# Kernel optimization log

Measured on AMD Instinct MI355X. Metric: run time of the kernel, lower is better.

The kernel has to match this reference:

```python
import jax, jax.numpy as jnp
import numpy as np

B = 50000      # batch of graphs
NOBJ = 7       # tangram pieces per graph
HID = 64
EMB = 32
SIGMA = 25.0   # VE-SDE sigma for marginal_prob_std


def _lin_init(k, fin, fout):
    kw, kb = jax.random.split(k)
    s = 1.0 / np.sqrt(fin)
    w = jax.random.uniform(kw, (fin, fout), minval=-s, maxval=s, dtype=jnp.float32)
    b = jax.random.uniform(kb, (fout,), minval=-s, maxval=s, dtype=jnp.float32)
    return w, b


def setup_inputs() -> dict:
    key = jax.random.key(0)
    ks = jax.random.split(key, 16)
    N = B * NOBJ
    omega = jax.random.normal(ks[0], (N, 3), dtype=jnp.float32)
    t = jax.random.uniform(ks[1], (B, 1), minval=1e-3, maxval=1.0, dtype=jnp.float32)
    # fully-connected edges (no self loops) per graph, offset by graph index
    a, b = np.meshgrid(np.arange(NOBJ), np.arange(NOBJ), indexing='ij')
    m = a != b
    src0, dst0 = a[m], b[m]                       # (42,)
    offs = (np.arange(B) * NOBJ)[:, None]         # (B,1)
    src = (src0[None, :] + offs).reshape(-1)
    dst = (dst0[None, :] + offs).reshape(-1)
    edge_index = jnp.asarray(np.stack([src, dst]), dtype=jnp.int32)  # (2, B*42)
    W_fourier = jax.random.normal(ks[2], (EMB // 2,), dtype=jnp.float32) * 30.0
    wi1, bi1 = _lin_init(ks[3], 3, HID)
    wi2, bi2 = _lin_init(ks[4], HID, HID)
    wt, bt = _lin_init(ks[5], EMB, EMB)
    w1a, b1a = _lin_init(ks[6], HID * 2, HID)
    w1b, b1b = _lin_init(ks[7], HID, HID)
    w2a, b2a = _lin_init(ks[8], (HID + EMB) * 2, HID)
    w2b, b2b = _lin_init(ks[9], HID, HID)
    w3a, b3a = _lin_init(ks[10], (HID + EMB) * 2, HID)
    w3b, b3b = _lin_init(ks[11], HID, 3)
    return dict(omega=omega, edge_index=edge_index, t=t, num_objs=NOBJ,
                W_fourier=W_fourier,
                wi1=wi1, bi1=bi1, wi2=wi2, bi2=bi2, wt=wt, bt=bt,
                w1a=w1a, b1a=b1a, w1b=w1b, b1b=b1b,
                w2a=w2a, b2a=b2a, w2b=w2b, b2b=b2b,
                w3a=w3a, b3a=b3a, w3b=w3b, b3b=b3b)


def _mlp(x, wa, ba, wb, bb):
    return jax.nn.relu(x @ wa + ba) @ wb + bb


def reference(omega, edge_index, t, num_objs, W_fourier,
              wi1, bi1, wi2, bi2, wt, bt,
              w1a, b1a, w1b, b1b, w2a, b2a, w2b, b2b, w3a, b3a, w3b, b3b):
    N = omega.shape[0]
    src, dst = edge_index[0], edge_index[1]

    def edge_conv(x, wa, ba, wb, bb):
        # EdgeConv: msg = mlp([x_i, x_j - x_i]); max-aggregate at target i
        xi = x[dst]
        msg = _mlp(jnp.concatenate([xi, x[src] - xi], axis=-1), wa, ba, wb, bb)
        return jax.ops.segment_max(msg, dst, num_segments=N)

    init_feature = _mlp(omega, wi1, bi1, wi2, bi2)          # (N, HID)
    # Gaussian Fourier time embedding -> ReLU -> Linear -> ReLU
    proj = t[:, 0][:, None] * W_fourier[None, :] * (2.0 * jnp.pi)   # (B, EMB/2)
    emb = jnp.concatenate([jnp.sin(proj), jnp.cos(proj)], axis=-1)  # (B, EMB)
    xs = jax.nn.relu(jax.nn.relu(emb) @ wt + bt)                    # (B, EMB)
    # torch: xs.repeat(1, num_objs, 1).view(B*num_objs, -1) == tile whole block
    x_sigma = jnp.tile(xs, (num_objs, 1))                           # (N, EMB)

    x = jax.nn.relu(edge_conv(init_feature, w1a, b1a, w1b, b1b))
    x = jnp.concatenate([x, x_sigma], axis=-1)
    x = jax.nn.relu(edge_conv(x, w2a, b2a, w2b, b2b))
    x = jnp.concatenate([x, x_sigma], axis=-1)
    x = edge_conv(x, w3a, b3a, w3b, b3b)                            # (N, 3)

    # torch: t.repeat(1, num_objs).view(B*num_objs, -1) == repeat_interleave
    t_r = jnp.repeat(t, num_objs, axis=0)                           # (N, 1)
    std = jnp.sqrt((SIGMA ** (2.0 * t_r) - 1.0) / (2.0 * jnp.log(SIGMA)))
    return x / (std + 1e-7)
```

## Files before the change

kernel.cpp:

```cpp
#include <hip/hip_runtime.h>


#define NB 50000

typedef unsigned short u16;
typedef short short8 __attribute__((ext_vector_type(8)));
typedef float f32x4 __attribute__((ext_vector_type(4)));

#define OFF_I  0
#define OFF_1A 8192
#define OFF_2A 24576
#define OFF_3A 49152
#define OFF_1B 73728
#define OFF_2B 81920
#define OFF_WT 90112
#define OFF_3B 92160

#define HSTR 144
#define HLO  2304
#define XS2S 72
#define XS2LO 1152
#define SSTR 264
#define WREG 11136

__device__ __forceinline__ float b2f(u16 u) {
    return __uint_as_float(((unsigned int)u) << 16);
}
__device__ __forceinline__ u16 f2b(float f) {
    unsigned int u = __float_as_uint(f);
    u += 0x7FFFu + ((u >> 16) & 1u);
    return (u16)(u >> 16);
}
__device__ __forceinline__ float bcast(float v, int l) {
    return __uint_as_float(__builtin_amdgcn_readlane(__float_as_uint(v), l));
}

__global__ __launch_bounds__(128) void pack_kernel(
    const float* __restrict__ wi2, const float* __restrict__ w1a,
    const float* __restrict__ w2a, const float* __restrict__ w3a,
    const float* __restrict__ w1b, const float* __restrict__ w2b,
    const float* __restrict__ wt,  const float* __restrict__ w3b,
    u16* __restrict__ ws)
{
    int blk = blockIdx.x;
    int half = threadIdx.x >> 6;
    int lane = threadIdx.x & 63;
    if (blk < 88) {
        const float* src; int NT, qoff, obase, frag;
        if (blk < 8)       { src = wi2; NT = 4; qoff = 0;  obase = OFF_I;  frag = blk;      }
        else if (blk < 24) { src = w1a; NT = 8; qoff = 64; obase = OFF_1A; frag = blk - 8;  }
        else if (blk < 48) { src = w2a; NT = 8; qoff = 96; obase = OFF_2A; frag = blk - 24; }
        else if (blk < 72) { src = w3a; NT = 8; qoff = 96; obase = OFF_3A; frag = blk - 48; }
        else if (blk < 80) { src = w1b; NT = 4; qoff = 0;  obase = OFF_1B; frag = blk - 72; }
        else               { src = w2b; NT = 4; qoff = 0;  obase = OFF_2B; frag = blk - 80; }
        int kt = frag / NT, nt = frag % NT;
        int k0 = kt * 32 + (lane >> 4) * 8;
        int n  = nt * 16 + (lane & 15);
        u16* dst = ws + obase + frag * 1024 + half * 512 + lane * 8;
#pragma unroll
        for (int j = 0; j < 8; ++j) {
            int k = k0 + j;
            int idx = (n < 64) ? (k * 64 + n) : ((qoff + k) * 64 + (n - 64));
            float v = src[idx];
            u16 hi = f2b(v);
            dst[j] = (half == 0) ? hi : f2b(v - b2f(hi));
        }
    } else if (blk < 90) {
        int frag = blk - 88;
        int k0 = (lane >> 4) * 8;
        int n  = frag * 16 + (lane & 15);
        u16* dst = ws + OFF_WT + frag * 1024 + half * 512 + lane * 8;
#pragma unroll
        for (int j = 0; j < 8; ++j) {
            float v = wt[(k0 + j) * 32 + n];
            u16 hi = f2b(v);
            dst[j] = (half == 0) ? hi : f2b(v - b2f(hi));
        }
    } else {
        int frag = blk - 90;
        int k0 = frag * 32 + (lane >> 4) * 8;
        int n  = lane & 15;
        u16* dst = ws + OFF_3B + frag * 1024 + half * 512 + lane * 8;
#pragma unroll
        for (int j = 0; j < 8; ++j) {
            float v = (n < 3) ? w3b[(k0 + j) * 3 + n] : 0.f;
            u16 hi = f2b(v);
            dst[j] = (half == 0) ? hi : f2b(v - b2f(hi));
        }
    }
}

__device__ __forceinline__ f32x4 mfma3(short8 ah, short8 al, short8 bh, short8 bl, f32x4 acc) {
    acc = __builtin_amdgcn_mfma_f32_16x16x32_bf16(ah, bh, acc, 0, 0, 0);
    acc = __builtin_amdgcn_mfma_f32_16x16x32_bf16(ah, bl, acc, 0, 0, 0);
    acc = __builtin_amdgcn_mfma_f32_16x16x32_bf16(al, bh, acc, 0, 0, 0);
    return acc;
}

#define ROW(k) ((k) < 7 ? (k) : (k) + 1)

__device__ __forceinline__ void writeX64_14(char* W, int L, const float* v) {
#pragma unroll
    for (int k = 0; k < 14; ++k) {
        int r = ROW(k);
        u16 hi = f2b(v[k]);
        *(u16*)(W + r * HSTR + L * 2) = hi;
        *(u16*)(W + HLO + r * HSTR + L * 2) = f2b(v[k] - b2f(hi));
    }
}
template<int KT>
__device__ __forceinline__ void loadA(const char* W, const char* XS2, int L,
                                      short8* Ah, short8* Al) {
#pragma unroll
    for (int kt = 0; kt < KT; ++kt) {
        if (kt < 2) {
            Ah[kt] = *(const short8*)(W + (L & 15) * HSTR + kt * 64 + (L >> 4) * 16);
            Al[kt] = *(const short8*)(W + HLO + (L & 15) * HSTR + kt * 64 + (L >> 4) * 16);
        } else {
            Ah[kt] = *(const short8*)(XS2 + (L & 15) * XS2S + (L >> 4) * 16);
            Al[kt] = *(const short8*)(XS2 + XS2LO + (L & 15) * XS2S + (L >> 4) * 16);
        }
    }
}
template<int KT, int NT>
__device__ __forceinline__ void lin_pass(const u16* __restrict__ ws, int off, int nt0,
                                         const short8* Ah, const short8* Al,
                                         char* Sb, int L) {
#pragma unroll
    for (int ntc = 0; ntc < 4; ++ntc) {
        f32x4 acc = {0.f, 0.f, 0.f, 0.f};
#pragma unroll
        for (int kt = 0; kt < KT; ++kt) {
            int f = kt * NT + nt0 + ntc;
            short8 bh = *(const short8*)(ws + off + f * 1024 + L * 8);
            short8 bl = *(const short8*)(ws + off + f * 1024 + 512 + L * 8);
            acc = mfma3(Ah[kt], Al[kt], bh, bl, acc);
        }
#pragma unroll
        for (int rr = 0; rr < 4; ++rr)
            *(float*)(Sb + ((L >> 4) * 4 + rr) * SSTR + ntc * 64 + (L & 15) * 4) = acc[rr];
    }
}
__device__ __forceinline__ void readS14(const char* Sb, int L, float* o) {
#pragma unroll
    for (int k = 0; k < 14; ++k) o[k] = *(const float*)(Sb + ROW(k) * SSTR + L * 4);
}
__device__ __forceinline__ void stageH2(char* W, int c, const float* pp, const float* qq, int L) {
#pragma unroll
    for (int r = 0; r < 16; ++r) {
        int e = c * 16 + r;
        if (e < 84) {
            int gb = (e >= 42) ? 1 : 0;
            int el = e - gb * 42;
            int i = el / 6, jj = el - i * 6;
            int j = jj + (jj >= i);
            float hv = fmaxf(pp[gb * 7 + i] + qq[gb * 7 + j], 0.f);
            u16 hi = f2b(hv);
            *(u16*)(W + r * HSTR + L * 2) = hi;
            *(u16*)(W + HLO + r * HSTR + L * 2) = f2b(hv - b2f(hi));
        }
    }
}
__device__ __forceinline__ void loadAH(const char* W, int L,
                                       short8& Ah0, short8& Ah1, short8& Al0, short8& Al1) {
    Ah0 = *(const short8*)(W + (L & 15) * HSTR + (L >> 4) * 16);
    Ah1 = *(const short8*)(W + (L & 15) * HSTR + 64 + (L >> 4) * 16);
    Al0 = *(const short8*)(W + HLO + (L & 15) * HSTR + (L >> 4) * 16);
    Al1 = *(const short8*)(W + HLO + (L & 15) * HSTR + 64 + (L >> 4) * 16);
}

__device__ __forceinline__ void edgeconv2(const u16* __restrict__ ws, int offB,
                                          char* W, char* Sb,
                                          const float* pp, const float* qq,
                                          float vb, int L) {
    float mx[14];
#pragma unroll
    for (int k = 0; k < 14; ++k) mx[k] = -3.0e38f;
#pragma unroll
    for (int c = 0; c < 6; ++c) {
        stageH2(W, c, pp, qq, L);
        short8 Ah0, Ah1, Al0, Al1;
        loadAH(W, L, Ah0, Ah1, Al0, Al1);
#pragma unroll
        for (int nt = 0; nt < 4; ++nt) {
            short8 bh0 = *(const short8*)(ws + offB + nt * 1024 + L * 8);
            short8 bl0 = *(const short8*)(ws + offB + nt * 1024 + 512 + L * 8);
            short8 bh1 = *(const short8*)(ws + offB + (4 + nt) * 1024 + L * 8);
            short8 bl1 = *(const short8*)(ws + offB + (4 + nt) * 1024 + 512 + L * 8);
            f32x4 acc = {0.f, 0.f, 0.f, 0.f};
            acc = mfma3(Ah0, Al0, bh0, bl0, acc);
            acc = mfma3(Ah1, Al1, bh1, bl1, acc);
#pragma unroll
            for (int rr = 0; rr < 4; ++rr)
                *(float*)(Sb + ((L >> 4) * 4 + rr) * SSTR + nt * 64 + (L & 15) * 4) = acc[rr];
        }
#pragma unroll
        for (int r = 0; r < 16; ++r) {
            int e = c * 16 + r;
            if (e < 84) {
                int gb = (e >= 42) ? 1 : 0;
                int i = (e - gb * 42) / 6;
                float sv = *(const float*)(Sb + r * SSTR + L * 4);
                mx[gb * 7 + i] = fmaxf(mx[gb * 7 + i], sv);
            }
        }
    }
    float xo[14];
#pragma unroll
    for (int k = 0; k < 14; ++k) xo[k] = fmaxf(mx[k] + vb, 0.f);
    writeX64_14(W, L, xo);
}

__global__ __launch_bounds__(128) void gnn_kernel(
    const float* __restrict__ omega, const float* __restrict__ tt, const float* __restrict__ Wf,
    const float* __restrict__ wi1, const float* __restrict__ bi1, const float* __restrict__ bi2,
    const float* __restrict__ bt,
    const float* __restrict__ b1a, const float* __restrict__ b1b,
    const float* __restrict__ b2a, const float* __restrict__ b2b,
    const float* __restrict__ b3a, const float* __restrict__ b3b,
    const u16* __restrict__ ws, float* __restrict__ out)
{
    __shared__ __align__(16) char smem[2 * WREG];
    const int L   = threadIdx.x & 63;
    const int wav = threadIdx.x >> 6;
    const int p   = blockIdx.x * 2 + wav;
    const int g0  = p * 2;
    const int base0 = g0 * 7;
    char* W   = smem + wav * WREG;
    char* XS2 = W + 4608;
    char* Sb  = W + 6912;

    float omv = (L < 42) ? omega[base0 * 3 + L] : 0.f;
    float vwi10 = wi1[L], vwi11 = wi1[64 + L], vwi12 = wi1[128 + L];
    float vbi1 = bi1[L];
    float h1[14];
#pragma unroll
    for (int k = 0; k < 14; ++k) {
        float a0 = bcast(omv, 3 * k), a1 = bcast(omv, 3 * k + 1), a2 = bcast(omv, 3 * k + 2);
        h1[k] = fmaxf(fmaf(a0, vwi10, fmaf(a1, vwi11, fmaf(a2, vwi12, vbi1))), 0.f);
    }

    {
        int cc = L & 31;
        float vwf = Wf[cc & 15] * 6.283185307179586f;
        int tb = base0 - (base0 / NB) * NB;
#pragma unroll
        for (int k = 0; k < 14; ++k) {
            int ti = tb + k; if (ti >= NB) ti -= NB;
            float pj = tt[ti] * vwf;
            float remb = fmaxf((cc < 16) ? sinf(pj) : cosf(pj), 0.f);
            u16 hi = f2b(remb);
            if (L < 32) *(u16*)(W + ROW(k) * HSTR + cc * 2) = hi;
            else *(u16*)(W + HLO + ROW(k) * HSTR + cc * 2) = f2b(remb - b2f(hi));
        }
        short8 Eh = *(const short8*)(W + (L & 15) * HSTR + (L >> 4) * 16);
        short8 El = *(const short8*)(W + HLO + (L & 15) * HSTR + (L >> 4) * 16);
#pragma unroll
        for (int nt = 0; nt < 2; ++nt) {
            short8 bh = *(const short8*)(ws + OFF_WT + nt * 1024 + L * 8);
            short8 bl = *(const short8*)(ws + OFF_WT + nt * 1024 + 512 + L * 8);
            f32x4 acc = {0.f, 0.f, 0.f, 0.f};
            acc = mfma3(Eh, El, bh, bl, acc);
#pragma unroll
            for (int rr = 0; rr < 4; ++rr)
                *(float*)(Sb + ((L >> 4) * 4 + rr) * SSTR + nt * 64 + (L & 15) * 4) = acc[rr];
        }
        float vbt = bt[cc];
#pragma unroll
        for (int k = 0; k < 14; ++k) {
            float xv = fmaxf(*(const float*)(Sb + ROW(k) * SSTR + cc * 4) + vbt, 0.f);
            u16 hi = f2b(xv);
            if (L < 32) *(u16*)(XS2 + ROW(k) * XS2S + cc * 2) = hi;
            else *(u16*)(XS2 + XS2LO + ROW(k) * XS2S + cc * 2) = f2b(xv - b2f(hi));
        }
    }

    short8 Ah[3], Al[3];
    float pp[14], qq[14];

    writeX64_14(W, L, h1);
    loadA<2>(W, XS2, L, Ah, Al);
    lin_pass<2, 4>(ws, OFF_I, 0, Ah, Al, Sb, L);
    {
        float xh[14];
        readS14(Sb, L, xh);
        float vbi2 = bi2[L];
#pragma unroll
        for (int k = 0; k < 14; ++k) xh[k] += vbi2;
        writeX64_14(W, L, xh);
    }

    loadA<2>(W, XS2, L, Ah, Al);
    lin_pass<2, 8>(ws, OFF_1A, 0, Ah, Al, Sb, L);
    readS14(Sb, L, pp);
    lin_pass<2, 8>(ws, OFF_1A, 4, Ah, Al, Sb, L);
    readS14(Sb, L, qq);
    float vb1a = b1a[L];
#pragma unroll
    for (int k = 0; k < 14; ++k) pp[k] = pp[k] + vb1a - qq[k];
    edgeconv2(ws, OFF_1B, W, Sb, pp, qq, b1b[L], L);

    loadA<3>(W, XS2, L, Ah, Al);
    lin_pass<3, 8>(ws, OFF_2A, 0, Ah, Al, Sb, L);
    readS14(Sb, L, pp);
    lin_pass<3, 8>(ws, OFF_2A, 4, Ah, Al, Sb, L);
    readS14(Sb, L, qq);
    float vb2a = b2a[L];
#pragma unroll
    for (int k = 0; k < 14; ++k) pp[k] = pp[k] + vb2a - qq[k];
    edgeconv2(ws, OFF_2B, W, Sb, pp, qq, b2b[L], L);

    loadA<3>(W, XS2, L, Ah, Al);
    lin_pass<3, 8>(ws, OFF_3A, 0, Ah, Al, Sb, L);
    readS14(Sb, L, pp);
    lin_pass<3, 8>(ws, OFF_3A, 4, Ah, Al, Sb, L);
    readS14(Sb, L, qq);
    float vb3a = b3a[L];
#pragma unroll
    for (int k = 0; k < 14; ++k) pp[k] = pp[k] + vb3a - qq[k];

    {
        short8 B0h = *(const short8*)(ws + OFF_3B + L * 8);
        short8 B0l = *(const short8*)(ws + OFF_3B + 512 + L * 8);
        short8 B1h = *(const short8*)(ws + OFF_3B + 1024 + L * 8);
        short8 B1l = *(const short8*)(ws + OFF_3B + 1536 + L * 8);
#pragma unroll
        for (int c = 0; c < 6; ++c) {
            stageH2(W, c, pp, qq, L);
            short8 Ah0, Ah1, Al0, Al1;
            loadAH(W, L, Ah0, Ah1, Al0, Al1);
            f32x4 acc = {0.f, 0.f, 0.f, 0.f};
            acc = mfma3(Ah0, Al0, B0h, B0l, acc);
            acc = mfma3(Ah1, Al1, B1h, B1l, acc);
            if ((L & 15) < 3) {
#pragma unroll
                for (int rr = 0; rr < 4; ++rr)
                    *(float*)(Sb + (c * 16 + (L >> 4) * 4 + rr) * 16 + (L & 15) * 4) = acc[rr];
            }
        }
        if (L < 42) {
            int gb = (L >= 21) ? 1 : 0;
            int ll = L - gb * 21;
            int i = ll / 3, col = ll - i * 3;
            int e0 = gb * 42 + i * 6;
            float m = -3.0e38f;
#pragma unroll
            for (int e6 = 0; e6 < 6; ++e6)
                m = fmaxf(m, *(const float*)(Sb + (e0 + e6) * 16 + col * 4));
            m += b3b[col];
            float tg = tt[g0 + gb];
            float stdv = sqrtf((exp2f(tg * 9.287712379549448f) - 1.0f) * 0.15533740282828987f);
            out[base0 * 3 + L] = m / (stdv + 1e-7f);
        }
    }
}

extern "C" void kernel_launch(void* const* d_in, const int* in_sizes, int n_in,
                              void* d_out, int out_size, void* d_ws, size_t ws_size,
                              hipStream_t stream) {
    const float* omega = (const float*)d_in[0];
    const float* tt  = (const float*)d_in[2];
    const float* Wf  = (const float*)d_in[4];
    const float* wi1 = (const float*)d_in[5];
    const float* bi1 = (const float*)d_in[6];
    const float* wi2 = (const float*)d_in[7];
    const float* bi2 = (const float*)d_in[8];
    const float* wt  = (const float*)d_in[9];
    const float* bt  = (const float*)d_in[10];
    const float* w1a = (const float*)d_in[11];
    const float* b1a = (const float*)d_in[12];
    const float* w1b = (const float*)d_in[13];
    const float* b1b = (const float*)d_in[14];
    const float* w2a = (const float*)d_in[15];
    const float* b2a = (const float*)d_in[16];
    const float* w2b = (const float*)d_in[17];
    const float* b2b = (const float*)d_in[18];
    const float* w3a = (const float*)d_in[19];
    const float* b3a = (const float*)d_in[20];
    const float* w3b = (const float*)d_in[21];
    const float* b3b = (const float*)d_in[22];
    u16* ws = (u16*)d_ws;

    pack_kernel<<<dim3(92), dim3(128), 0, stream>>>(wi2, w1a, w2a, w3a, w1b, w2b, wt, w3b, ws);
    gnn_kernel<<<dim3(12500), dim3(128), 0, stream>>>(
        omega, tt, Wf, wi1, bi1, bi2, bt,
        b1a, b1b, b2a, b2b, b3a, b3b, ws, (float*)d_out);
}
```

Measured before the change: 487.3 us.

## Pad edge rows per node so segment-max reduces in registers via shuffles

```diff
diff --git a/kernel.cpp b/kernel.cpp
--- a/kernel.cpp
+++ b/kernel.cpp
@@ -18,10 +18,10 @@
 
 #define HSTR 144
 #define HLO  2304
+#define SSTR 276
 #define XS2S 72
 #define XS2LO 1152
-#define SSTR 264
-#define WREG 11136
+#define WREG 11520
 
 __device__ __forceinline__ float b2f(u16 u) {
     return __uint_as_float(((unsigned int)u) << 16);
@@ -99,23 +99,23 @@
 
 #define ROW(k) ((k) < 7 ? (k) : (k) + 1)
 
-__device__ __forceinline__ void writeX64_14(char* W, int L, const float* v) {
+__device__ __forceinline__ void writeX64_14(char* G, int L, const float* v) {
 #pragma unroll
     for (int k = 0; k < 14; ++k) {
         int r = ROW(k);
         u16 hi = f2b(v[k]);
-        *(u16*)(W + r * HSTR + L * 2) = hi;
-        *(u16*)(W + HLO + r * HSTR + L * 2) = f2b(v[k] - b2f(hi));
+        *(u16*)(G + r * HSTR + L * 2) = hi;
+        *(u16*)(G + HLO + r * HSTR + L * 2) = f2b(v[k] - b2f(hi));
     }
 }
 template<int KT>
-__device__ __forceinline__ void loadA(const char* W, const char* XS2, int L,
+__device__ __forceinline__ void loadA(const char* G, const char* XS2, int L,
                                       short8* Ah, short8* Al) {
 #pragma unroll
     for (int kt = 0; kt < KT; ++kt) {
         if (kt < 2) {
-            Ah[kt] = *(const short8*)(W + (L & 15) * HSTR + kt * 64 + (L >> 4) * 16);
-            Al[kt] = *(const short8*)(W + HLO + (L & 15) * HSTR + kt * 64 + (L >> 4) * 16);
+            Ah[kt] = *(const short8*)(G + (L & 15) * HSTR + kt * 64 + (L >> 4) * 16);
+            Al[kt] = *(const short8*)(G + HLO + (L & 15) * HSTR + kt * 64 + (L >> 4) * 16);
         } else {
             Ah[kt] = *(const short8*)(XS2 + (L & 15) * XS2S + (L >> 4) * 16);
             Al[kt] = *(const short8*)(XS2 + XS2LO + (L & 15) * XS2S + (L >> 4) * 16);
@@ -125,7 +125,7 @@
 template<int KT, int NT>
 __device__ __forceinline__ void lin_pass(const u16* __restrict__ ws, int off, int nt0,
                                          const short8* Ah, const short8* Al,
-                                         char* Sb, int L) {
+                                         char* Sg, int L) {
 #pragma unroll
     for (int ntc = 0; ntc < 4; ++ntc) {
         f32x4 acc = {0.f, 0.f, 0.f, 0.f};
@@ -138,49 +138,49 @@
         }
 #pragma unroll
         for (int rr = 0; rr < 4; ++rr)
-            *(float*)(Sb + ((L >> 4) * 4 + rr) * SSTR + ntc * 64 + (L & 15) * 4) = acc[rr];
-    }
-}
-__device__ __forceinline__ void readS14(const char* Sb, int L, float* o) {
-#pragma unroll
-    for (int k = 0; k < 14; ++k) o[k] = *(const float*)(Sb + ROW(k) * SSTR + L * 4);
-}
-__device__ __forceinline__ void stageH2(char* W, int c, const float* pp, const float* qq, int L) {
+            *(float*)(Sg + ((L >> 4) * 4 + rr) * SSTR + ntc * 64 + (L & 15) * 4) = acc[rr];
+    }
+}
+__device__ __forceinline__ void readS14(const char* Sg, int L, float* o) {
+#pragma unroll
+    for (int k = 0; k < 14; ++k) o[k] = *(const float*)(Sg + ROW(k) * SSTR + L * 4);
+}
+__device__ __forceinline__ void stageH2(char* G, int c, const float* pp, const float* qq, int L) {
 #pragma unroll
     for (int r = 0; r < 16; ++r) {
-        int e = c * 16 + r;
-        if (e < 84) {
-            int gb = (e >= 42) ? 1 : 0;
-            int el = e - gb * 42;
-            int i = el / 6, jj = el - i * 6;
-            int j = jj + (jj >= i);
-            float hv = fmaxf(pp[gb * 7 + i] + qq[gb * 7 + j], 0.f);
-            u16 hi = f2b(hv);
-            *(u16*)(W + r * HSTR + L * 2) = hi;
-            *(u16*)(W + HLO + r * HSTR + L * 2) = f2b(hv - b2f(hi));
-        }
-    }
-}
-__device__ __forceinline__ void loadAH(const char* W, int L,
+        int gidx = c * 2 + (r >> 3);
+        int gb = (gidx >= 7) ? 1 : 0;
+        int i = gidx - gb * 7;
+        int rg = r & 7;
+        int jj = (rg < 6) ? rg : 0;
+        int j = jj + (jj >= i);
+        float hv = fmaxf(pp[gb * 7 + i] + qq[gb * 7 + j], 0.f);
+        u16 hi = f2b(hv);
+        *(u16*)(G + r * HSTR + L * 2) = hi;
+        *(u16*)(G + HLO + r * HSTR + L * 2) = f2b(hv - b2f(hi));
+    }
+}
+__device__ __forceinline__ void loadAH(const char* G, int L,
                                        short8& Ah0, short8& Ah1, short8& Al0, short8& Al1) {
-    Ah0 = *(const short8*)(W + (L & 15) * HSTR + (L >> 4) * 16);
-    Ah1 = *(const short8*)(W + (L & 15) * HSTR + 64 + (L >> 4) * 16);
-    Al0 = *(const short8*)(W + HLO + (L & 15) * HSTR + (L >> 4) * 16);
-    Al1 = *(const short8*)(W + HLO + (L & 15) * HSTR + 64 + (L >> 4) * 16);
-}
-
-__device__ __forceinline__ void edgeconv2(const u16* __restrict__ ws, int offB,
-                                          char* W, char* Sb,
+    Ah0 = *(const short8*)(G + (L & 15) * HSTR + (L >> 4) * 16);
+    Ah1 = *(const short8*)(G + (L & 15) * HSTR + 64 + (L >> 4) * 16);
+    Al0 = *(const short8*)(G + HLO + (L & 15) * HSTR + (L >> 4) * 16);
+    Al1 = *(const short8*)(G + HLO + (L & 15) * HSTR + 64 + (L >> 4) * 16);
+}
+
+__device__ __forceinline__ void edgeconv3(const u16* __restrict__ ws, int offB,
+                                          char* Ghreg, char* Gxout,
                                           const float* pp, const float* qq,
-                                          float vb, int L) {
-    float mx[14];
-#pragma unroll
-    for (int k = 0; k < 14; ++k) mx[k] = -3.0e38f;
-#pragma unroll
-    for (int c = 0; c < 6; ++c) {
-        stageH2(W, c, pp, qq, L);
+                                          const float* bb, int L) {
+    int q = L >> 4;
+#pragma unroll
+    for (int c = 0; c < 7; ++c) {
+        stageH2(Ghreg, c, pp, qq, L);
         short8 Ah0, Ah1, Al0, Al1;
-        loadAH(W, L, Ah0, Ah1, Al0, Al1);
+        loadAH(Ghreg, L, Ah0, Ah1, Al0, Al1);
+        int gidx = c * 2 + (q >> 1);
+        int gb = (gidx >= 7) ? 1 : 0;
+        int xrow = gidx + gb;
 #pragma unroll
         for (int nt = 0; nt < 4; ++nt) {
             short8 bh0 = *(const short8*)(ws + offB + nt * 1024 + L * 8);
@@ -190,25 +190,15 @@
             f32x4 acc = {0.f, 0.f, 0.f, 0.f};
             acc = mfma3(Ah0, Al0, bh0, bl0, acc);
             acc = mfma3(Ah1, Al1, bh1, bl1, acc);
-#pragma unroll
-            for (int rr = 0; rr < 4; ++rr)
-                *(float*)(Sb + ((L >> 4) * 4 + rr) * SSTR + nt * 64 + (L & 15) * 4) = acc[rr];
-        }
-#pragma unroll
-        for (int r = 0; r < 16; ++r) {
-            int e = c * 16 + r;
-            if (e < 84) {
-                int gb = (e >= 42) ? 1 : 0;
-                int i = (e - gb * 42) / 6;
-                float sv = *(const float*)(Sb + r * SSTR + L * 4);
-                mx[gb * 7 + i] = fmaxf(mx[gb * 7 + i], sv);
-            }
-        }
-    }
-    float xo[14];
-#pragma unroll
-    for (int k = 0; k < 14; ++k) xo[k] = fmaxf(mx[k] + vb, 0.f);
-    writeX64_14(W, L, xo);
+            float m = fmaxf(fmaxf(acc[0], acc[1]), fmaxf(acc[2], acc[3]));
+            m = fmaxf(m, __shfl_xor(m, 16, 64));
+            float xv = fmaxf(m + bb[nt], 0.f);
+            u16 hi = f2b(xv);
+            u16 w = (q & 1) ? f2b(xv - b2f(hi)) : hi;
+            int plane = (q & 1) ? HLO : 0;
+            *(u16*)(Gxout + plane + xrow * HSTR + (nt * 16 + (L & 15)) * 2) = w;
+        }
+    }
 }
 
 __global__ __launch_bounds__(128) void gnn_kernel(
@@ -226,9 +216,9 @@
     const int p   = blockIdx.x * 2 + wav;
     const int g0  = p * 2;
     const int base0 = g0 * 7;
-    char* W   = smem + wav * WREG;
-    char* XS2 = W + 4608;
-    char* Sb  = W + 6912;
+    char* G0  = smem + wav * WREG;
+    char* G1  = G0 + 4608;
+    char* XS2 = G0 + 9216;
 
     float omv = (L < 42) ? omega[base0 * 3 + L] : 0.f;
     float vwi10 = wi1[L], vwi11 = wi1[64 + L], vwi12 = wi1[128 + L];
@@ -250,11 +240,11 @@
             float pj = tt[ti] * vwf;
             float remb = fmaxf((cc < 16) ? sinf(pj) : cosf(pj), 0.f);
             u16 hi = f2b(remb);
-            if (L < 32) *(u16*)(W + ROW(k) * HSTR + cc * 2) = hi;
-            else *(u16*)(W + HLO + ROW(k) * HSTR + cc * 2) = f2b(remb - b2f(hi));
-        }
-        short8 Eh = *(const short8*)(W + (L & 15) * HSTR + (L >> 4) * 16);
-        short8 El = *(const short8*)(W + HLO + (L & 15) * HSTR + (L >> 4) * 16);
+            if (L < 32) *(u16*)(G0 + ROW(k) * HSTR + cc * 2) = hi;
+            else *(u16*)(G0 + HLO + ROW(k) * HSTR + cc * 2) = f2b(remb - b2f(hi));
+        }
+        short8 Eh = *(const short8*)(G0 + (L & 15) * HSTR + (L >> 4) * 16);
+        short8 El = *(const short8*)(G0 + HLO + (L & 15) * HSTR + (L >> 4) * 16);
 #pragma unroll
         for (int nt = 0; nt < 2; ++nt) {
             short8 bh = *(const short8*)(ws + OFF_WT + nt * 1024 + L * 8);
@@ -263,12 +253,12 @@
             acc = mfma3(Eh, El, bh, bl, acc);
 #pragma unroll
             for (int rr = 0; rr < 4; ++rr)
-                *(float*)(Sb + ((L >> 4) * 4 + rr) * SSTR + nt * 64 + (L & 15) * 4) = acc[rr];
+                *(float*)(G1 + ((L >> 4) * 4 + rr) * SSTR + nt * 64 + (L & 15) * 4) = acc[rr];
         }
         float vbt = bt[cc];
 #pragma unroll
         for (int k = 0; k < 14; ++k) {
-            float xv = fmaxf(*(const float*)(Sb + ROW(k) * SSTR + cc * 4) + vbt, 0.f);
+            float xv = fmaxf(*(const float*)(G1 + ROW(k) * SSTR + cc * 4) + vbt, 0.f);
             u16 hi = f2b(xv);
             if (L < 32) *(u16*)(XS2 + ROW(k) * XS2S + cc * 2) = hi;
             else *(u16*)(XS2 + XS2LO + ROW(k) * XS2S + cc * 2) = f2b(xv - b2f(hi));
@@ -278,43 +268,53 @@
     short8 Ah[3], Al[3];
     float pp[14], qq[14];
 
-    writeX64_14(W, L, h1);
-    loadA<2>(W, XS2, L, Ah, Al);
-    lin_pass<2, 4>(ws, OFF_I, 0, Ah, Al, Sb, L);
+    writeX64_14(G0, L, h1);
+    loadA<2>(G0, XS2, L, Ah, Al);
+    lin_pass<2, 4>(ws, OFF_I, 0, Ah, Al, G1, L);
     {
         float xh[14];
-        readS14(Sb, L, xh);
+        readS14(G1, L, xh);
         float vbi2 = bi2[L];
 #pragma unroll
         for (int k = 0; k < 14; ++k) xh[k] += vbi2;
-        writeX64_14(W, L, xh);
-    }
-
-    loadA<2>(W, XS2, L, Ah, Al);
-    lin_pass<2, 8>(ws, OFF_1A, 0, Ah, Al, Sb, L);
-    readS14(Sb, L, pp);
-    lin_pass<2, 8>(ws, OFF_1A, 4, Ah, Al, Sb, L);
-    readS14(Sb, L, qq);
+        writeX64_14(G0, L, xh);
+    }
+
+    loadA<2>(G0, XS2, L, Ah, Al);
+    lin_pass<2, 8>(ws, OFF_1A, 0, Ah, Al, G1, L);
+    readS14(G1, L, pp);
+    lin_pass<2, 8>(ws, OFF_1A, 4, Ah, Al, G1, L);
+    readS14(G1, L, qq);
     float vb1a = b1a[L];
 #pragma unroll
     for (int k = 0; k < 14; ++k) pp[k] = pp[k] + vb1a - qq[k];
-    edgeconv2(ws, OFF_1B, W, Sb, pp, qq, b1b[L], L);
-
-    loadA<3>(W, XS2, L, Ah, Al);
-    lin_pass<3, 8>(ws, OFF_2A, 0, Ah, Al, Sb, L);
-    readS14(Sb, L, pp);
-    lin_pass<3, 8>(ws, OFF_2A, 4, Ah, Al, Sb, L);
-    readS14(Sb, L, qq);
+    {
+        float bb[4];
+#pragma unroll
+        for (int nt = 0; nt < 4; ++nt) bb[nt] = b1b[nt * 16 + (L & 15)];
+        edgeconv3(ws, OFF_1B, G0, G1, pp, qq, bb, L);
+    }
+
+    loadA<3>(G1, XS2, L, Ah, Al);
+    lin_pass<3, 8>(ws, OFF_2A, 0, Ah, Al, G0, L);
+    readS14(G0, L, pp);
+    lin_pass<3, 8>(ws, OFF_2A, 4, Ah, Al, G0, L);
+    readS14(G0, L, qq);
     float vb2a = b2a[L];
 #pragma unroll
     for (int k = 0; k < 14; ++k) pp[k] = pp[k] + vb2a - qq[k];
-    edgeconv2(ws, OFF_2B, W, Sb, pp, qq, b2b[L], L);
-
-    loadA<3>(W, XS2, L, Ah, Al);
-    lin_pass<3, 8>(ws, OFF_3A, 0, Ah, Al, Sb, L);
-    readS14(Sb, L, pp);
-    lin_pass<3, 8>(ws, OFF_3A, 4, Ah, Al, Sb, L);
-    readS14(Sb, L, qq);
+    {
+        float bb[4];
+#pragma unroll
+        for (int nt = 0; nt < 4; ++nt) bb[nt] = b2b[nt * 16 + (L & 15)];
+        edgeconv3(ws, OFF_2B, G1, G0, pp, qq, bb, L);
+    }
+
+    loadA<3>(G0, XS2, L, Ah, Al);
+    lin_pass<3, 8>(ws, OFF_3A, 0, Ah, Al, G1, L);
+    readS14(G1, L, pp);
+    lin_pass<3, 8>(ws, OFF_3A, 4, Ah, Al, G1, L);
+    readS14(G1, L, qq);
     float vb3a = b3a[L];
 #pragma unroll
     for (int k = 0; k < 14; ++k) pp[k] = pp[k] + vb3a - qq[k];
@@ -324,33 +324,27 @@
         short8 B0l = *(const short8*)(ws + OFF_3B + 512 + L * 8);
         short8 B1h = *(const short8*)(ws + OFF_3B + 1024 + L * 8);
         short8 B1l = *(const short8*)(ws + OFF_3B + 1536 + L * 8);
-#pragma unroll
-        for (int c = 0; c < 6; ++c) {
-            stageH2(W, c, pp, qq, L);
+        float t0 = tt[g0], t1 = tt[g0 + 1];
+        float inv0 = 1.0f / (sqrtf((exp2f(t0 * 9.287712379549448f) - 1.0f) * 0.15533740282828987f) + 1e-7f);
+        float inv1 = 1.0f / (sqrtf((exp2f(t1 * 9.287712379549448f) - 1.0f) * 0.15533740282828987f) + 1e-7f);
+        float vb3b = b3b[(L & 15) < 3 ? (L & 15) : 0];
+        int q = L >> 4;
+#pragma unroll
+        for (int c = 0; c < 7; ++c) {
+            stageH2(G0, c, pp, qq, L);
             short8 Ah0, Ah1, Al0, Al1;
-            loadAH(W, L, Ah0, Ah1, Al0, Al1);
+            loadAH(G0, L, Ah0, Ah1, Al0, Al1);
             f32x4 acc = {0.f, 0.f, 0.f, 0.f};
             acc = mfma3(Ah0, Al0, B0h, B0l, acc);
             acc = mfma3(Ah1, Al1, B1h, B1l, acc);
-            if ((L & 15) < 3) {
-#pragma unroll
-                for (int rr = 0; rr < 4; ++rr)
-                    *(float*)(Sb + (c * 16 + (L >> 4) * 4 + rr) * 16 + (L & 15) * 4) = acc[rr];
+            float m = fmaxf(fmaxf(acc[0], acc[1]), fmaxf(acc[2], acc[3]));
+            m = fmaxf(m, __shfl_xor(m, 16, 64));
+            int gidx = c * 2 + (q >> 1);
+            int gb = (gidx >= 7) ? 1 : 0;
+            if ((L & 15) < 3 && !(q & 1)) {
+                float v = (m + vb3b) * (gb ? inv1 : inv0);
+                out[(base0 + gidx) * 3 + (L & 15)] = v;
             }
-        }
-        if (L < 42) {
-            int gb = (L >= 21) ? 1 : 0;
-            int ll = L - gb * 21;
-            int i = ll / 3, col = ll - i * 3;
-            int e0 = gb * 42 + i * 6;
-            float m = -3.0e38f;
-#pragma unroll
-            for (int e6 = 0; e6 < 6; ++e6)
-                m = fmaxf(m, *(const float*)(Sb + (e0 + e6) * 16 + col * 4));
-            m += b3b[col];
-            float tg = tt[g0 + gb];
-            float stdv = sqrtf((exp2f(tg * 9.287712379549448f) - 1.0f) * 0.15533740282828987f);
-            out[base0 * 3 + L] = m / (stdv + 1e-7f);
         }
     }
 }
```

Result: slower. 562.8 us (+15.5%).

## Double-buffer edge staging and split MFMA accumulators to overlap LDS and matrix work

Applied to the files above, without the earlier changes.

```diff
diff --git a/kernel.cpp b/kernel.cpp
--- a/kernel.cpp
+++ b/kernel.cpp
@@ -21,7 +21,7 @@
 #define XS2S 72
 #define XS2LO 1152
 #define SSTR 264
-#define WREG 11136
+#define WREG 15744
 
 __device__ __forceinline__ float b2f(u16 u) {
     return __uint_as_float(((unsigned int)u) << 16);
@@ -90,32 +90,35 @@
     }
 }
 
+__device__ __forceinline__ f32x4 mfma1(short8 a, short8 b, f32x4 acc) {
+    return __builtin_amdgcn_mfma_f32_16x16x32_bf16(a, b, acc, 0, 0, 0);
+}
 __device__ __forceinline__ f32x4 mfma3(short8 ah, short8 al, short8 bh, short8 bl, f32x4 acc) {
-    acc = __builtin_amdgcn_mfma_f32_16x16x32_bf16(ah, bh, acc, 0, 0, 0);
-    acc = __builtin_amdgcn_mfma_f32_16x16x32_bf16(ah, bl, acc, 0, 0, 0);
-    acc = __builtin_amdgcn_mfma_f32_16x16x32_bf16(al, bh, acc, 0, 0, 0);
+    acc = mfma1(ah, bh, acc);
+    acc = mfma1(ah, bl, acc);
+    acc = mfma1(al, bh, acc);
     return acc;
 }
 
 #define ROW(k) ((k) < 7 ? (k) : (k) + 1)
 
-__device__ __forceinline__ void writeX64_14(char* W, int L, const float* v) {
+__device__ __forceinline__ void writeX64_14(char* G, int L, const float* v) {
 #pragma unroll
     for (int k = 0; k < 14; ++k) {
         int r = ROW(k);
         u16 hi = f2b(v[k]);
-        *(u16*)(W + r * HSTR + L * 2) = hi;
-        *(u16*)(W + HLO + r * HSTR + L * 2) = f2b(v[k] - b2f(hi));
+        *(u16*)(G + r * HSTR + L * 2) = hi;
+        *(u16*)(G + HLO + r * HSTR + L * 2) = f2b(v[k] - b2f(hi));
     }
 }
 template<int KT>
-__device__ __forceinline__ void loadA(const char* W, const char* XS2, int L,
+__device__ __forceinline__ void loadA(const char* G, const char* XS2, int L,
                                       short8* Ah, short8* Al) {
 #pragma unroll
     for (int kt = 0; kt < KT; ++kt) {
         if (kt < 2) {
-            Ah[kt] = *(const short8*)(W + (L & 15) * HSTR + kt * 64 + (L >> 4) * 16);
-            Al[kt] = *(const short8*)(W + HLO + (L & 15) * HSTR + kt * 64 + (L >> 4) * 16);
+            Ah[kt] = *(const short8*)(G + (L & 15) * HSTR + kt * 64 + (L >> 4) * 16);
+            Al[kt] = *(const short8*)(G + HLO + (L & 15) * HSTR + kt * 64 + (L >> 4) * 16);
         } else {
             Ah[kt] = *(const short8*)(XS2 + (L & 15) * XS2S + (L >> 4) * 16);
             Al[kt] = *(const short8*)(XS2 + XS2LO + (L & 15) * XS2S + (L >> 4) * 16);
@@ -125,27 +128,29 @@
 template<int KT, int NT>
 __device__ __forceinline__ void lin_pass(const u16* __restrict__ ws, int off, int nt0,
                                          const short8* Ah, const short8* Al,
-                                         char* Sb, int L) {
+                                         char* Sg, int L) {
 #pragma unroll
     for (int ntc = 0; ntc < 4; ++ntc) {
-        f32x4 acc = {0.f, 0.f, 0.f, 0.f};
+        f32x4 a1 = {0.f, 0.f, 0.f, 0.f}, a2 = {0.f, 0.f, 0.f, 0.f};
 #pragma unroll
         for (int kt = 0; kt < KT; ++kt) {
             int f = kt * NT + nt0 + ntc;
             short8 bh = *(const short8*)(ws + off + f * 1024 + L * 8);
             short8 bl = *(const short8*)(ws + off + f * 1024 + 512 + L * 8);
-            acc = mfma3(Ah[kt], Al[kt], bh, bl, acc);
+            a1 = mfma1(Ah[kt], bh, a1);
+            a2 = mfma1(Ah[kt], bl, a2);
+            a2 = mfma1(Al[kt], bh, a2);
         }
 #pragma unroll
         for (int rr = 0; rr < 4; ++rr)
-            *(float*)(Sb + ((L >> 4) * 4 + rr) * SSTR + ntc * 64 + (L & 15) * 4) = acc[rr];
-    }
-}
-__device__ __forceinline__ void readS14(const char* Sb, int L, float* o) {
-#pragma unroll
-    for (int k = 0; k < 14; ++k) o[k] = *(const float*)(Sb + ROW(k) * SSTR + L * 4);
-}
-__device__ __forceinline__ void stageH2(char* W, int c, const float* pp, const float* qq, int L) {
+            *(float*)(Sg + ((L >> 4) * 4 + rr) * SSTR + ntc * 64 + (L & 15) * 4) = a1[rr] + a2[rr];
+    }
+}
+__device__ __forceinline__ void readS14(const char* Sg, int L, float* o) {
+#pragma unroll
+    for (int k = 0; k < 14; ++k) o[k] = *(const float*)(Sg + ROW(k) * SSTR + L * 4);
+}
+__device__ __forceinline__ void stageH2(char* G, int c, const float* pp, const float* qq, int L) {
 #pragma unroll
     for (int r = 0; r < 16; ++r) {
         int e = c * 16 + r;
@@ -156,55 +161,66 @@
             int j = jj + (jj >= i);
             float hv = fmaxf(pp[gb * 7 + i] + qq[gb * 7 + j], 0.f);
             u16 hi = f2b(hv);
-            *(u16*)(W + r * HSTR + L * 2) = hi;
-            *(u16*)(W + HLO + r * HSTR + L * 2) = f2b(hv - b2f(hi));
-        }
-    }
-}
-__device__ __forceinline__ void loadAH(const char* W, int L,
+            *(u16*)(G + r * HSTR + L * 2) = hi;
+            *(u16*)(G + HLO + r * HSTR + L * 2) = f2b(hv - b2f(hi));
+        }
+    }
+}
+__device__ __forceinline__ void loadAH(const char* G, int L,
                                        short8& Ah0, short8& Ah1, short8& Al0, short8& Al1) {
-    Ah0 = *(const short8*)(W + (L & 15) * HSTR + (L >> 4) * 16);
-    Ah1 = *(const short8*)(W + (L & 15) * HSTR + 64 + (L >> 4) * 16);
-    Al0 = *(const short8*)(W + HLO + (L & 15) * HSTR + (L >> 4) * 16);
-    Al1 = *(const short8*)(W + HLO + (L & 15) * HSTR + 64 + (L >> 4) * 16);
-}
-
-__device__ __forceinline__ void edgeconv2(const u16* __restrict__ ws, int offB,
-                                          char* W, char* Sb,
-                                          const float* pp, const float* qq,
-                                          float vb, int L) {
+    Ah0 = *(const short8*)(G + (L & 15) * HSTR + (L >> 4) * 16);
+    Ah1 = *(const short8*)(G + (L & 15) * HSTR + 64 + (L >> 4) * 16);
+    Al0 = *(const short8*)(G + HLO + (L & 15) * HSTR + (L >> 4) * 16);
+    Al1 = *(const short8*)(G + HLO + (L & 15) * HSTR + 64 + (L >> 4) * 16);
+}
+__device__ __forceinline__ void maxread(const char* Sb, int cc, float* mx, int L) {
+#pragma unroll
+    for (int r = 0; r < 16; ++r) {
+        int e = cc * 16 + r;
+        if (e < 84) {
+            int gb = (e >= 42) ? 1 : 0;
+            int i = (e - gb * 42) / 6;
+            float sv = *(const float*)(Sb + r * SSTR + L * 4);
+            mx[gb * 7 + i] = fmaxf(mx[gb * 7 + i], sv);
+        }
+    }
+}
+
+__device__ __forceinline__ void edgeconv_pipe(const u16* __restrict__ ws, int offB,
+                                              char* W, char* H1, char* Sb,
+                                              const float* pp, const float* qq,
+                                              float vb, int L) {
     float mx[14];
 #pragma unroll
     for (int k = 0; k < 14; ++k) mx[k] = -3.0e38f;
+    stageH2(W, 0, pp, qq, L);
+    short8 Ah0, Ah1, Al0, Al1;
+    loadAH(W, L, Ah0, Ah1, Al0, Al1);
 #pragma unroll
     for (int c = 0; c < 6; ++c) {
-        stageH2(W, c, pp, qq, L);
-        short8 Ah0, Ah1, Al0, Al1;
-        loadAH(W, L, Ah0, Ah1, Al0, Al1);
+        char* Hn = ((c + 1) & 1) ? H1 : W;
+        if (c < 5) stageH2(Hn, c + 1, pp, qq, L);
+        if (c > 0) maxread(Sb, c - 1, mx, L);
 #pragma unroll
         for (int nt = 0; nt < 4; ++nt) {
             short8 bh0 = *(const short8*)(ws + offB + nt * 1024 + L * 8);
             short8 bl0 = *(const short8*)(ws + offB + nt * 1024 + 512 + L * 8);
             short8 bh1 = *(const short8*)(ws + offB + (4 + nt) * 1024 + L * 8);
             short8 bl1 = *(const short8*)(ws + offB + (4 + nt) * 1024 + 512 + L * 8);
-            f32x4 acc = {0.f, 0.f, 0.f, 0.f};
-            acc = mfma3(Ah0, Al0, bh0, bl0, acc);
-            acc = mfma3(Ah1, Al1, bh1, bl1, acc);
+            f32x4 a1 = {0.f, 0.f, 0.f, 0.f}, a2 = {0.f, 0.f, 0.f, 0.f};
+            a1 = mfma1(Ah0, bh0, a1);
+            a2 = mfma1(Ah0, bl0, a2);
+            a2 = mfma1(Al0, bh0, a2);
+            a1 = mfma1(Ah1, bh1, a1);
+            a2 = mfma1(Ah1, bl1, a2);
+            a2 = mfma1(Al1, bh1, a2);
 #pragma unroll
             for (int rr = 0; rr < 4; ++rr)
-                *(float*)(Sb + ((L >> 4) * 4 + rr) * SSTR + nt * 64 + (L & 15) * 4) = acc[rr];
-        }
-#pragma unroll
-        for (int r = 0; r < 16; ++r) {
-            int e = c * 16 + r;
-            if (e < 84) {
-                int gb = (e >= 42) ? 1 : 0;
-                int i = (e - gb * 42) / 6;
-                float sv = *(const float*)(Sb + r * SSTR + L * 4);
-                mx[gb * 7 + i] = fmaxf(mx[gb * 7 + i], sv);
-            }
-        }
-    }
+                *(float*)(Sb + ((L >> 4) * 4 + rr) * SSTR + nt * 64 + (L & 15) * 4) = a1[rr] + a2[rr];
+        }
+        if (c < 5) loadAH(Hn, L, Ah0, Ah1, Al0, Al1);
+    }
+    maxread(Sb, 5, mx, L);
     float xo[14];
 #pragma unroll
     for (int k = 0; k < 14; ++k) xo[k] = fmaxf(mx[k] + vb, 0.f);
@@ -228,7 +244,8 @@
     const int base0 = g0 * 7;
     char* W   = smem + wav * WREG;
     char* XS2 = W + 4608;
-    char* Sb  = W + 6912;
+    char* H1  = W + 6912;
+    char* Sb  = W + 11520;
 
     float omv = (L < 42) ? omega[base0 * 3 + L] : 0.f;
     float vwi10 = wi1[L], vwi11 = wi1[64 + L], vwi12 = wi1[128 + L];
@@ -248,7 +265,7 @@
         for (int k = 0; k < 14; ++k) {
             int ti = tb + k; if (ti >= NB) ti -= NB;
             float pj = tt[ti] * vwf;
-            float remb = fmaxf((cc < 16) ? sinf(pj) : cosf(pj), 0.f);
+            float remb = fmaxf((cc < 16) ? __sinf(pj) : __cosf(pj), 0.f);
             u16 hi = f2b(remb);
             if (L < 32) *(u16*)(W + ROW(k) * HSTR + cc * 2) = hi;
             else *(u16*)(W + HLO + ROW(k) * HSTR + cc * 2) = f2b(remb - b2f(hi));
@@ -298,7 +315,7 @@
     float vb1a = b1a[L];
 #pragma unroll
     for (int k = 0; k < 14; ++k) pp[k] = pp[k] + vb1a - qq[k];
-    edgeconv2(ws, OFF_1B, W, Sb, pp, qq, b1b[L], L);
+    edgeconv_pipe(ws, OFF_1B, W, H1, Sb, pp, qq, b1b[L], L);
 
     loadA<3>(W, XS2, L, Ah, Al);
     lin_pass<3, 8>(ws, OFF_2A, 0, Ah, Al, Sb, L);
@@ -308,7 +325,7 @@
     float vb2a = b2a[L];
 #pragma unroll
     for (int k = 0; k < 14; ++k) pp[k] = pp[k] + vb2a - qq[k];
-    edgeconv2(ws, OFF_2B, W, Sb, pp, qq, b2b[L], L);
+    edgeconv_pipe(ws, OFF_2B, W, H1, Sb, pp, qq, b2b[L], L);
 
     loadA<3>(W, XS2, L, Ah, Al);
     lin_pass<3, 8>(ws, OFF_3A, 0, Ah, Al, Sb, L);
@@ -324,19 +341,26 @@
         short8 B0l = *(const short8*)(ws + OFF_3B + 512 + L * 8);
         short8 B1h = *(const short8*)(ws + OFF_3B + 1024 + L * 8);
         short8 B1l = *(const short8*)(ws + OFF_3B + 1536 + L * 8);
+        stageH2(W, 0, pp, qq, L);
+        short8 Ah0, Ah1, Al0, Al1;
+        loadAH(W, L, Ah0, Ah1, Al0, Al1);
 #pragma unroll
         for (int c = 0; c < 6; ++c) {
-            stageH2(W, c, pp, qq, L);
-            short8 Ah0, Ah1, Al0, Al1;
-            loadAH(W, L, Ah0, Ah1, Al0, Al1);
-            f32x4 acc = {0.f, 0.f, 0.f, 0.f};
-            acc = mfma3(Ah0, Al0, B0h, B0l, acc);
-            acc = mfma3(Ah1, Al1, B1h, B1l, acc);
+            char* Hn = ((c + 1) & 1) ? H1 : W;
+            if (c < 5) stageH2(Hn, c + 1, pp, qq, L);
+            f32x4 a1 = {0.f, 0.f, 0.f, 0.f}, a2 = {0.f, 0.f, 0.f, 0.f};
+            a1 = mfma1(Ah0, B0h, a1);
+            a2 = mfma1(Ah0, B0l, a2);
+            a2 = mfma1(Al0, B0h, a2);
+            a1 = mfma1(Ah1, B1h, a1);
+            a2 = mfma1(Ah1, B1l, a2);
+            a2 = mfma1(Al1, B1h, a2);
             if ((L & 15) < 3) {
 #pragma unroll
                 for (int rr = 0; rr < 4; ++rr)
-                    *(float*)(Sb + (c * 16 + (L >> 4) * 4 + rr) * 16 + (L & 15) * 4) = acc[rr];
+                    *(float*)(Sb + (c * 16 + (L >> 4) * 4 + rr) * 16 + (L & 15) * 4) = a1[rr] + a2[rr];
             }
+            if (c < 5) loadAH(Hn, L, Ah0, Ah1, Al0, Al1);
         }
         if (L < 42) {
             int gb = (L >= 21) ? 1 : 0;
```

Result: faster. 451.9 us (-7.3%).
